# Kernel optimization log

Measured on AMD Instinct MI355X. Metric: run time of the kernel, lower is better.

The kernel has to match this reference:

```python
import jax, jax.numpy as jnp
import numpy as np

N_USERS = 100000
N_ITEMS = 50000
N = N_USERS + N_ITEMS + 2   # concat of user (+pad) and item (+pad) embedding tables
D = 128                      # embedding_size
E = 600000                   # edges per behavior adjacency
L = 2                        # GCN layers per (post, pre) behavior pair
EPS = 1e-12                  # F.normalize eps


def setup_inputs() -> dict:
    key = jax.random.key(0)
    ks = jax.random.split(key, 11)
    emb = jax.random.normal(ks[0], (N, D), jnp.float32) * 0.1
    rows_aux = jax.random.randint(ks[1], (E,), 0, N, jnp.int32)
    cols_aux = jax.random.randint(ks[2], (E,), 0, N, jnp.int32)
    vals_aux = jax.random.uniform(ks[3], (E,), jnp.float32)
    rows_buy = jax.random.randint(ks[4], (E,), 0, N, jnp.int32)
    cols_buy = jax.random.randint(ks[5], (E,), 0, N, jnp.int32)
    vals_buy = jax.random.uniform(ks[6], (E,), jnp.float32)
    trans_aux_all = jax.random.uniform(ks[7], (N, 1), jnp.float32)
    trans_buy_all = jax.random.uniform(ks[8], (N, 1), jnp.float32)
    trans_buy_aux = jax.random.uniform(ks[9], (N, 1), jnp.float32)
    # precomputed edge-dropout masks (keep_rate ~ 0.5 via 0/1 randint), one per SpMM layer call
    masks = jax.random.randint(ks[10], (6, E), 0, 2, jnp.int32).astype(bool)
    return {
        "emb": emb,
        "rows_aux": rows_aux, "cols_aux": cols_aux, "vals_aux": vals_aux,
        "rows_buy": rows_buy, "cols_buy": cols_buy, "vals_buy": vals_buy,
        "trans_aux_all": trans_aux_all,
        "trans_buy_all": trans_buy_all,
        "trans_buy_aux": trans_buy_aux,
        "masks": masks,
    }


def _spmm(rows, cols, vals, x):
    # sparse [N,N] @ dense [N,D] in COO form: gather source rows, scale, scatter-add to dest rows
    return jax.ops.segment_sum(vals[:, None] * x[cols], rows, num_segments=N)


def _gcn(x, rows, cols, vals, layer_masks):
    acc = x
    for l in range(L):
        x = _spmm(rows, cols, vals * layer_masks[l], x)
        acc = acc + x
    return acc / (L + 1)


def _l2norm(x):
    n = jnp.linalg.norm(x, axis=-1, keepdims=True)
    return x / jnp.maximum(n, EPS)


def reference(emb, rows_aux, cols_aux, vals_aux, rows_buy, cols_buy, vals_buy,
              trans_aux_all, trans_buy_all, trans_buy_aux, masks):
    m = masks.astype(emb.dtype)  # dropped edges contribute 0 == removing them from the COO tensor
    last = emb
    # behavior 'aux': pre-behaviors = ['all']
    g = _gcn(emb, rows_aux, cols_aux, vals_aux, m[0:2])
    agg = trans_aux_all * g
    cur_aux = _l2norm(agg) + last
    last = cur_aux
    # behavior 'buy': pre-behaviors = ['all', 'aux'] (reversed order; sum is order-invariant)
    g_all = _gcn(emb, rows_buy, cols_buy, vals_buy, m[2:4])
    g_aux = _gcn(cur_aux, rows_buy, cols_buy, vals_buy, m[4:6])
    agg = trans_buy_all * g_all + trans_buy_aux * g_aux
    cur_buy = _l2norm(agg) + last
    return cur_buy
```

## Files before the change

### kernel.cpp

```cpp
#include <hip/hip_runtime.h>
#include <cstdint>
#include <cstddef>

#define NNODES 150002
#define NN2    (2 * NNODES)
#define DIM    128
#define NEDGE  600000
#define EPSN   1e-12f


__global__ void hist_both(const int* __restrict__ ra,
                          const int* __restrict__ rb,
                          int* __restrict__ cnt)
{
    int e = blockIdx.x * blockDim.x + threadIdx.x;
    if (e < NEDGE)           atomicAdd(&cnt[ra[e]], 1);
    else if (e < 2 * NEDGE)  atomicAdd(&cnt[NNODES + rb[e - NEDGE]], 1);
}

__global__ __launch_bounds__(1024)
void scan_phase1(const int* __restrict__ cnt,
                 int* __restrict__ local,
                 int* __restrict__ partials)
{
    __shared__ int lds[1024];
    int t = threadIdx.x;
    int i = blockIdx.x * 1024 + t;
    int v = (i < NN2) ? cnt[i] : 0;
    lds[t] = v;
    __syncthreads();
    for (int off = 1; off < 1024; off <<= 1) {
        int w = (t >= off) ? lds[t - off] : 0;
        __syncthreads();
        lds[t] += w;
        __syncthreads();
    }
    if (i < NN2) local[i] = lds[t] - v;
    if (t == 1023) partials[blockIdx.x] = lds[1023];
}

__global__ __launch_bounds__(512)
void scan_phase2(int* __restrict__ partials, int nparts)
{
    __shared__ int lds[512];
    int t = threadIdx.x;
    int v = (t < nparts) ? partials[t] : 0;
    lds[t] = v;
    __syncthreads();
    for (int off = 1; off < 512; off <<= 1) {
        int w = (t >= off) ? lds[t - off] : 0;
        __syncthreads();
        lds[t] += w;
        __syncthreads();
    }
    if (t < nparts) partials[t] = lds[t] - v;
}

__global__ __launch_bounds__(1024)
void scan_phase3(int* __restrict__ rp,
                 const int* __restrict__ partials,
                 int* __restrict__ cursor)
{
    int i = blockIdx.x * 1024 + threadIdx.x;
    if (i >= NN2) return;
    int v = rp[i] + partials[blockIdx.x];
    rp[i] = v;
    cursor[i] = v;
    if (i == 0) rp[NN2] = 2 * NEDGE;
}

__global__ void scatter_both(const int* __restrict__ ra, const int* __restrict__ ca,
                             const float* __restrict__ va,
                             const int* __restrict__ rb, const int* __restrict__ cb,
                             const float* __restrict__ vb,
                             const int* __restrict__ masks,
                             int* __restrict__ cursor,
                             uint2* __restrict__ ent)
{
    int e = blockIdx.x * blockDim.x + threadIdx.x;
    if (e < NEDGE) {
        unsigned bits = (masks[e] != 0 ? 1u : 0u)
                      | (masks[(size_t)NEDGE + e] != 0 ? 2u : 0u);
        int pos = atomicAdd(&cursor[ra[e]], 1);
        ent[pos] = make_uint2((unsigned)ca[e] | (bits << 24), __float_as_uint(va[e]));
    } else if (e < 2 * NEDGE) {
        int e2 = e - NEDGE;
        unsigned bits = 0;
#pragma unroll
        for (int k = 0; k < 4; ++k)
            bits |= (masks[(size_t)(2 + k) * NEDGE + e2] != 0 ? 1u : 0u) << k;
        int pos = atomicAdd(&cursor[NNODES + rb[e2]], 1);
        ent[pos] = make_uint2((unsigned)cb[e2] | (bits << 24), __float_as_uint(vb[e2]));
    }
}

#define G16_SETUP                                              \
    int gid  = blockIdx.x * blockDim.x + threadIdx.x;          \
    int row  = gid >> 4;                                       \
    int lane = gid & 15;                                       \
    if (row >= NNODES) return;                                 \
    size_t base = (size_t)row * DIM + lane * 4;

#define FMA4(acc, v, xv)                                       \
    acc.x = fmaf(v, xv.x, acc.x);                              \
    acc.y = fmaf(v, xv.y, acc.y);                              \
    acc.z = fmaf(v, xv.z, acc.z);                              \
    acc.w = fmaf(v, xv.w, acc.w);

#define ADD4(a, b) a.x += b.x; a.y += b.y; a.z += b.z; a.w += b.w;

__device__ __forceinline__ void gather16_1(const int* __restrict__ rp,
                                           const uint2* __restrict__ ent,
                                           unsigned bm, int row, int lane,
                                           const float* __restrict__ x,
                                           float4& alo, float4& ahi)
{
    int j0 = rp[row], j1 = rp[row + 1];
    float4 l0 = {0,0,0,0}, h0 = {0,0,0,0}, l1 = {0,0,0,0}, h1 = {0,0,0,0};
    int j = j0;
    for (; j + 2 <= j1; j += 2) {
        uint2 Ea = ent[j], Eb = ent[j + 1];
        bool ma = (Ea.x & bm) != 0, mb = (Eb.x & bm) != 0;
        const float* pa = x + (size_t)(Ea.x & 0xFFFFFFu) * DIM + lane * 4;
        const float* pb = x + (size_t)(Eb.x & 0xFFFFFFu) * DIM + lane * 4;
        float4 xla, xha, xlb, xhb;
        if (ma) { xla = *(const float4*)pa;        xha = *(const float4*)(pa + 64); }
        if (mb) { xlb = *(const float4*)pb;        xhb = *(const float4*)(pb + 64); }
        if (ma) { float v = __uint_as_float(Ea.y); FMA4(l0, v, xla) FMA4(h0, v, xha) }
        if (mb) { float v = __uint_as_float(Eb.y); FMA4(l1, v, xlb) FMA4(h1, v, xhb) }
    }
    if (j < j1) {
        uint2 E = ent[j];
        if ((E.x & bm) != 0) {
            const float* p = x + (size_t)(E.x & 0xFFFFFFu) * DIM + lane * 4;
            float v = __uint_as_float(E.y);
            float4 xl = *(const float4*)p, xh = *(const float4*)(p + 64);
            FMA4(l0, v, xl) FMA4(h0, v, xh)
        }
    }
    ADD4(l0, l1) ADD4(h0, h1)
    alo = l0; ahi = h0;
}

__device__ __forceinline__ void gather16_2(const int* __restrict__ rp,
                                           const uint2* __restrict__ ent,
                                           int row, int lane,
                                           const float* __restrict__ xA, unsigned bmA,
                                           const float* __restrict__ xB, unsigned bmB,
                                           float4& Alo, float4& Ahi,
                                           float4& Blo, float4& Bhi)
{
    int j0 = rp[row], j1 = rp[row + 1];
    float4 al0 = {0,0,0,0}, ah0 = {0,0,0,0}, al1 = {0,0,0,0}, ah1 = {0,0,0,0};
    float4 bl0 = {0,0,0,0}, bh0 = {0,0,0,0}, bl1 = {0,0,0,0}, bh1 = {0,0,0,0};
    int j = j0;
    for (; j + 2 <= j1; j += 2) {
        uint2 Ea = ent[j], Eb = ent[j + 1];
        size_t ca = (size_t)(Ea.x & 0xFFFFFFu) * DIM + lane * 4;
        size_t cb = (size_t)(Eb.x & 0xFFFFFFu) * DIM + lane * 4;
        bool maA = (Ea.x & bmA) != 0, maB = (Ea.x & bmB) != 0;
        bool mbA = (Eb.x & bmA) != 0, mbB = (Eb.x & bmB) != 0;
        float4 xaAl, xaAh, xaBl, xaBh, xbAl, xbAh, xbBl, xbBh;
        if (maA) { xaAl = *(const float4*)(xA + ca); xaAh = *(const float4*)(xA + ca + 64); }
        if (maB) { xaBl = *(const float4*)(xB + ca); xaBh = *(const float4*)(xB + ca + 64); }
        if (mbA) { xbAl = *(const float4*)(xA + cb); xbAh = *(const float4*)(xA + cb + 64); }
        if (mbB) { xbBl = *(const float4*)(xB + cb); xbBh = *(const float4*)(xB + cb + 64); }
        float va = __uint_as_float(Ea.y), vb = __uint_as_float(Eb.y);
        if (maA) { FMA4(al0, va, xaAl) FMA4(ah0, va, xaAh) }
        if (maB) { FMA4(bl0, va, xaBl) FMA4(bh0, va, xaBh) }
        if (mbA) { FMA4(al1, vb, xbAl) FMA4(ah1, vb, xbAh) }
        if (mbB) { FMA4(bl1, vb, xbBl) FMA4(bh1, vb, xbBh) }
    }
    if (j < j1) {
        uint2 E = ent[j];
        size_t cc = (size_t)(E.x & 0xFFFFFFu) * DIM + lane * 4;
        bool mA = (E.x & bmA) != 0, mB = (E.x & bmB) != 0;
        float4 xAl, xAh, xBl, xBh;
        if (mA) { xAl = *(const float4*)(xA + cc); xAh = *(const float4*)(xA + cc + 64); }
        if (mB) { xBl = *(const float4*)(xB + cc); xBh = *(const float4*)(xB + cc + 64); }
        float v = __uint_as_float(E.y);
        if (mA) { FMA4(al0, v, xAl) FMA4(ah0, v, xAh) }
        if (mB) { FMA4(bl0, v, xBl) FMA4(bh0, v, xBh) }
    }
    ADD4(al0, al1) ADD4(ah0, ah1) ADD4(bl0, bl1) ADD4(bh0, bh1)
    Alo = al0; Ahi = ah0; Blo = bl0; Bhi = bh0;
}

__global__ void aux1_kernel(const int* __restrict__ rp, const uint2* __restrict__ ent,
                            const float* __restrict__ emb, float* __restrict__ B0)
{
    G16_SETUP
    float4 alo, ahi;
    gather16_1(rp, ent, 1u << 24, row, lane, emb, alo, ahi);
    *reinterpret_cast<float4*>(B0 + base)      = alo;
    *reinterpret_cast<float4*>(B0 + base + 64) = ahi;
}

__global__ void aux2_kernel(const int* __restrict__ rp, const uint2* __restrict__ ent,
                            const float* __restrict__ B0, const float* __restrict__ emb,
                            const float* __restrict__ trans, float* __restrict__ out)
{
    G16_SETUP
    float4 alo, ahi;
    gather16_1(rp, ent, 1u << 25, row, lane, B0, alo, ahi);
    float t = trans[row] * (1.0f / 3.0f);
    float4 elo = *reinterpret_cast<const float4*>(emb + base);
    float4 ehi = *reinterpret_cast<const float4*>(emb + base + 64);
    float4 blo = *reinterpret_cast<const float4*>(B0 + base);
    float4 bhi = *reinterpret_cast<const float4*>(B0 + base + 64);
    float4 lo, hi;
    lo.x = t * (elo.x + blo.x + alo.x); lo.y = t * (elo.y + blo.y + alo.y);
    lo.z = t * (elo.z + blo.z + alo.z); lo.w = t * (elo.w + blo.w + alo.w);
    hi.x = t * (ehi.x + bhi.x + ahi.x); hi.y = t * (ehi.y + bhi.y + ahi.y);
    hi.z = t * (ehi.z + bhi.z + ahi.z); hi.w = t * (ehi.w + bhi.w + ahi.w);
    float ss = lo.x*lo.x + lo.y*lo.y + lo.z*lo.z + lo.w*lo.w
             + hi.x*hi.x + hi.y*hi.y + hi.z*hi.z + hi.w*hi.w;
#pragma unroll
    for (int off = 8; off > 0; off >>= 1) ss += __shfl_xor(ss, off, 64);
    float inv = 1.0f / fmaxf(sqrtf(ss), EPSN);
    float4 olo, ohi;
    olo.x = lo.x * inv + elo.x; olo.y = lo.y * inv + elo.y;
    olo.z = lo.z * inv + elo.z; olo.w = lo.w * inv + elo.w;
    ohi.x = hi.x * inv + ehi.x; ohi.y = hi.y * inv + ehi.y;
    ohi.z = hi.z * inv + ehi.z; ohi.w = hi.w * inv + ehi.w;
    *reinterpret_cast<float4*>(out + base)      = olo;
    *reinterpret_cast<float4*>(out + base + 64) = ohi;
}

__global__ void buy1_kernel(const int* __restrict__ rp, const uint2* __restrict__ ent,
                            const float* __restrict__ emb, const float* __restrict__ cur,
                            float* __restrict__ B0, float* __restrict__ B1)
{
    G16_SETUP
    float4 Alo, Ahi, Xlo, Xhi;
    gather16_2(rp, ent, row, lane, emb, 1u << 24, cur, 1u << 26, Alo, Ahi, Xlo, Xhi);
    *reinterpret_cast<float4*>(B0 + base)      = Alo;
    *reinterpret_cast<float4*>(B0 + base + 64) = Ahi;
    *reinterpret_cast<float4*>(B1 + base)      = Xlo;
    *reinterpret_cast<float4*>(B1 + base + 64) = Xhi;
}

__global__ void buy2_kernel(const int* __restrict__ rp, const uint2* __restrict__ ent,
                            const float* __restrict__ B0, const float* __restrict__ B1,
                            const float* __restrict__ emb,
                            const float* __restrict__ tall, const float* __restrict__ taux,
                            float* __restrict__ out)
{
    G16_SETUP
    float4 Alo, Ahi, Xlo, Xhi;
    gather16_2(rp, ent, row, lane, B0, 1u << 25, B1, 1u << 27, Alo, Ahi, Xlo, Xhi);
    float ta = tall[row] * (1.0f / 3.0f);
    float tx = taux[row] * (1.0f / 3.0f);
    float4 elo = *reinterpret_cast<const float4*>(emb + base);
    float4 ehi = *reinterpret_cast<const float4*>(emb + base + 64);
    float4 clo = *reinterpret_cast<const float4*>(out + base);
    float4 chi = *reinterpret_cast<const float4*>(out + base + 64);
    float4 b0lo = *reinterpret_cast<const float4*>(B0 + base);
    float4 b0hi = *reinterpret_cast<const float4*>(B0 + base + 64);
    float4 b1lo = *reinterpret_cast<const float4*>(B1 + base);
    float4 b1hi = *reinterpret_cast<const float4*>(B1 + base + 64);
    float4 lo, hi;
    lo.x = ta * (elo.x + b0lo.x + Alo.x) + tx * (clo.x + b1lo.x + Xlo.x);
    lo.y = ta * (elo.y + b0lo.y + Alo.y) + tx * (clo.y + b1lo.y + Xlo.y);
    lo.z = ta * (elo.z + b0lo.z + Alo.z) + tx * (clo.z + b1lo.z + Xlo.z);
    lo.w = ta * (elo.w + b0lo.w + Alo.w) + tx * (clo.w + b1lo.w + Xlo.w);
    hi.x = ta * (ehi.x + b0hi.x + Ahi.x) + tx * (chi.x + b1hi.x + Xhi.x);
    hi.y = ta * (ehi.y + b0hi.y + Ahi.y) + tx * (chi.y + b1hi.y + Xhi.y);
    hi.z = ta * (ehi.z + b0hi.z + Ahi.z) + tx * (chi.z + b1hi.z + Xhi.z);
    hi.w = ta * (ehi.w + b0hi.w + Ahi.w) + tx * (chi.w + b1hi.w + Xhi.w);
    float ss = lo.x*lo.x + lo.y*lo.y + lo.z*lo.z + lo.w*lo.w
             + hi.x*hi.x + hi.y*hi.y + hi.z*hi.z + hi.w*hi.w;
#pragma unroll
    for (int off = 8; off > 0; off >>= 1) ss += __shfl_xor(ss, off, 64);
    float inv = 1.0f / fmaxf(sqrtf(ss), EPSN);
    float4 olo, ohi;
    olo.x = lo.x * inv + clo.x; olo.y = lo.y * inv + clo.y;
    olo.z = lo.z * inv + clo.z; olo.w = lo.w * inv + clo.w;
    ohi.x = hi.x * inv + chi.x; ohi.y = hi.y * inv + chi.y;
    ohi.z = hi.z * inv + chi.z; ohi.w = hi.w * inv + chi.w;
    *reinterpret_cast<float4*>(out + base)      = olo;
    *reinterpret_cast<float4*>(out + base + 64) = ohi;
}

__global__ void spmm_kernel(const int* __restrict__ rows, const int* __restrict__ cols,
                            const float* __restrict__ vals, const int* __restrict__ mask,
                            const float* __restrict__ x, float* __restrict__ y)
{
    long long gid = (long long)blockIdx.x * blockDim.x + threadIdx.x;
    int e = (int)(gid >> 5); int lane = (int)(gid & 31);
    if (e >= NEDGE) return;
    if (!mask[e]) return;
    float v = vals[e]; int c = cols[e]; int r = rows[e];
    float4 xv = *reinterpret_cast<const float4*>(x + (size_t)c * DIM + lane * 4);
    float* dst = y + (size_t)r * DIM + lane * 4;
    atomicAdd(dst + 0, v * xv.x); atomicAdd(dst + 1, v * xv.y);
    atomicAdd(dst + 2, v * xv.z); atomicAdd(dst + 3, v * xv.w);
}

__global__ void spmm_scaled_kernel(const int* __restrict__ rows, const int* __restrict__ cols,
                                   const float* __restrict__ vals, const int* __restrict__ mask,
                                   const float* __restrict__ x, float* __restrict__ y,
                                   const float* __restrict__ rowscale)
{
    long long gid = (long long)blockIdx.x * blockDim.x + threadIdx.x;
    int e = (int)(gid >> 5); int lane = (int)(gid & 31);
    if (e >= NEDGE) return;
    if (!mask[e]) return;
    int r = rows[e];
    float v = vals[e] * rowscale[r] * (1.0f / 3.0f);
    int c = cols[e];
    float4 xv = *reinterpret_cast<const float4*>(x + (size_t)c * DIM + lane * 4);
    float* dst = y + (size_t)r * DIM + lane * 4;
    atomicAdd(dst + 0, v * xv.x); atomicAdd(dst + 1, v * xv.y);
    atomicAdd(dst + 2, v * xv.z); atomicAdd(dst + 3, v * xv.w);
}

__global__ void rownorm_aux_kernel(const float* __restrict__ emb, const float* __restrict__ s,
                                   const float* __restrict__ trans, float* __restrict__ out)
{
    int gid = blockIdx.x * blockDim.x + threadIdx.x;
    int row = gid >> 6; int lane = gid & 63;
    if (row >= NNODES) return;
    float t = trans[row] * (1.0f / 3.0f);
    size_t base = (size_t)row * DIM + lane * 2;
    float2 e  = *reinterpret_cast<const float2*>(emb + base);
    float2 sv = *reinterpret_cast<const float2*>(s + base);
    float ax = t * (e.x + sv.x); float ay = t * (e.y + sv.y);
    float ss = ax * ax + ay * ay;
#pragma unroll
    for (int off = 32; off > 0; off >>= 1) ss += __shfl_xor(ss, off, 64);
    float inv = 1.0f / fmaxf(sqrtf(ss), EPSN);
    float2 o; o.x = ax * inv + e.x; o.y = ay * inv + e.y;
    *reinterpret_cast<float2*>(out + base) = o;
}

__global__ void rownorm_final_kernel(const float* __restrict__ cur_aux, const float* __restrict__ b,
                                     const float* __restrict__ tbaux, float* __restrict__ out)
{
    int gid = blockIdx.x * blockDim.x + threadIdx.x;
    int row = gid >> 6; int lane = gid & 63;
    if (row >= NNODES) return;
    float t = tbaux[row] * (1.0f / 3.0f);
    size_t base = (size_t)row * DIM + lane * 2;
    float2 ca = *reinterpret_cast<const float2*>(cur_aux + base);
    float2 bv = *reinterpret_cast<const float2*>(b + base);
    float ax = bv.x + t * ca.x; float ay = bv.y + t * ca.y;
    float ss = ax * ax + ay * ay;
#pragma unroll
    for (int off = 32; off > 0; off >>= 1) ss += __shfl_xor(ss, off, 64);
    float inv = 1.0f / fmaxf(sqrtf(ss), EPSN);
    float2 o; o.x = ax * inv + ca.x; o.y = ay * inv + ca.y;
    *reinterpret_cast<float2*>(out + base) = o;
}

__global__ void combine_all_kernel(const float* __restrict__ emb, const float* __restrict__ tball,
                                   float* __restrict__ b)
{
    int i = blockIdx.x * blockDim.x + threadIdx.x;
    const int n4 = NNODES * DIM / 4;
    if (i >= n4) return;
    int row = i >> 5;
    float t = tball[row] * (1.0f / 3.0f);
    float4 e  = reinterpret_cast<const float4*>(emb)[i];
    float4 bv = reinterpret_cast<float4*>(b)[i];
    bv.x = t * (e.x + bv.x); bv.y = t * (e.y + bv.y);
    bv.z = t * (e.z + bv.z); bv.w = t * (e.w + bv.w);
    reinterpret_cast<float4*>(b)[i] = bv;
}

__global__ void add_scaled_kernel(const float* __restrict__ a, const float* __restrict__ tbaux,
                                  float* __restrict__ b)
{
    int i = blockIdx.x * blockDim.x + threadIdx.x;
    const int n4 = NNODES * DIM / 4;
    if (i >= n4) return;
    int row = i >> 5;
    float t = tbaux[row] * (1.0f / 3.0f);
    float4 av = reinterpret_cast<const float4*>(a)[i];
    float4 bv = reinterpret_cast<float4*>(b)[i];
    bv.x += t * av.x; bv.y += t * av.y; bv.z += t * av.z; bv.w += t * av.w;
    reinterpret_cast<float4*>(b)[i] = bv;
}

extern "C" void kernel_launch(void* const* d_in, const int* in_sizes, int n_in,
                              void* d_out, int out_size, void* d_ws, size_t ws_size,
                              hipStream_t stream)
{
    const float* emb       = (const float*)d_in[0];
    const int*   rows_aux  = (const int*)d_in[1];
    const int*   cols_aux  = (const int*)d_in[2];
    const float* vals_aux  = (const float*)d_in[3];
    const int*   rows_buy  = (const int*)d_in[4];
    const int*   cols_buy  = (const int*)d_in[5];
    const float* vals_buy  = (const float*)d_in[6];
    const float* t_aux_all = (const float*)d_in[7];
    const float* t_buy_all = (const float*)d_in[8];
    const float* t_buy_aux = (const float*)d_in[9];
    const int*   masks     = (const int*)d_in[10];

    float* out = (float*)d_out;
    const size_t nd = (size_t)NNODES * DIM;
    const size_t nd_bytes = nd * sizeof(float);

    uint8_t* wsb = (uint8_t*)d_ws;
    size_t off = 0;
    auto carve = [&](size_t bytes) -> void* {
        void* p = wsb + off;
        off = (off + bytes + 15) & ~(size_t)15;
        return p;
    };
    const int SCAN_BLOCKS = (NN2 + 1023) / 1024;
    float* B0       = (float*)carve(nd_bytes);
    float* B1       = (float*)carve(nd_bytes);
    uint2* ent      = (uint2*)carve((size_t)2 * NEDGE * 8);
    int*   rp       = (int*)carve(((size_t)NN2 + 1) * 4);
    int*   cursor   = (int*)carve((size_t)NN2 * 4);
    int*   cnt      = (int*)carve((size_t)NN2 * 4);
    int*   partials = (int*)carve((size_t)SCAN_BLOCKS * 4);
    const bool use_csr = (off <= ws_size);

    if (use_csr) {
        const int EB   = 256;
        const int EG2  = (2 * NEDGE + EB - 1) / EB;
        const int GB   = 256;
        const int GG   = (NNODES * 16 + GB - 1) / GB;

        hipMemsetAsync(cnt, 0, (size_t)NN2 * 4, stream);
        hist_both<<<EG2, EB, 0, stream>>>(rows_aux, rows_buy, cnt);
        scan_phase1<<<SCAN_BLOCKS, 1024, 0, stream>>>(cnt, rp, partials);
        scan_phase2<<<1, 512, 0, stream>>>(partials, SCAN_BLOCKS);
        scan_phase3<<<SCAN_BLOCKS, 1024, 0, stream>>>(rp, partials, cursor);
        scatter_both<<<EG2, EB, 0, stream>>>(rows_aux, cols_aux, vals_aux,
                                             rows_buy, cols_buy, vals_buy,
                                             masks, cursor, ent);

        aux1_kernel<<<GG, GB, 0, stream>>>(rp, ent, emb, B0);
        aux2_kernel<<<GG, GB, 0, stream>>>(rp, ent, B0, emb, t_aux_all, out);

        buy1_kernel<<<GG, GB, 0, stream>>>(rp + NNODES, ent, emb, out, B0, B1);
        buy2_kernel<<<GG, GB, 0, stream>>>(rp + NNODES, ent, B0, B1, emb,
                                           t_buy_all, t_buy_aux, out);
        return;
    }

    const int SPMM_BLK  = 256;
    const int SPMM_GRID = (int)(((long long)NEDGE * 32 + SPMM_BLK - 1) / SPMM_BLK);
    const int ROW_BLK   = 256;
    const int ROW_GRID  = (NNODES * 64 + ROW_BLK - 1) / ROW_BLK;
    const int EW_BLK    = 256;
    const int EW_GRID   = (int)((nd / 4 + EW_BLK - 1) / EW_BLK);

    hipMemsetAsync(B0, 0, nd_bytes, stream);
    spmm_kernel<<<SPMM_GRID, SPMM_BLK, 0, stream>>>(rows_aux, cols_aux, vals_aux,
                                                    masks + 0 * (size_t)NEDGE, emb, B0);
    hipMemcpyAsync(B1, B0, nd_bytes, hipMemcpyDeviceToDevice, stream);
    spmm_kernel<<<SPMM_GRID, SPMM_BLK, 0, stream>>>(rows_aux, cols_aux, vals_aux,
                                                    masks + 1 * (size_t)NEDGE, B0, B1);
    rownorm_aux_kernel<<<ROW_GRID, ROW_BLK, 0, stream>>>(emb, B1, t_aux_all, out);

    hipMemsetAsync(B0, 0, nd_bytes, stream);
    spmm_kernel<<<SPMM_GRID, SPMM_BLK, 0, stream>>>(rows_buy, cols_buy, vals_buy,
                                                    masks + 2 * (size_t)NEDGE, emb, B0);
    hipMemcpyAsync(B1, B0, nd_bytes, hipMemcpyDeviceToDevice, stream);
    spmm_kernel<<<SPMM_GRID, SPMM_BLK, 0, stream>>>(rows_buy, cols_buy, vals_buy,
                                                    masks + 3 * (size_t)NEDGE, B0, B1);
    combine_all_kernel<<<EW_GRID, EW_BLK, 0, stream>>>(emb, t_buy_all, B1);

    hipMemsetAsync(B0, 0, nd_bytes, stream);
    spmm_kernel<<<SPMM_GRID, SPMM_BLK, 0, stream>>>(rows_buy, cols_buy, vals_buy,
                                                    masks + 4 * (size_t)NEDGE, out, B0);
    add_scaled_kernel<<<EW_GRID, EW_BLK, 0, stream>>>(B0, t_buy_aux, B1);
    spmm_scaled_kernel<<<SPMM_GRID, SPMM_BLK, 0, stream>>>(rows_buy, cols_buy, vals_buy,
                                                           masks + 5 * (size_t)NEDGE, B0, B1,
                                                           t_buy_aux);
    rownorm_final_kernel<<<ROW_GRID, ROW_BLK, 0, stream>>>(out, B1, t_buy_aux, out);
}
```

Before: 531.1 us.

## Store gathered embeddings and intermediates in bf16 to halve gather traffic

Adds a kernel that converts the embedding table to bf16, and stores the intermediate layer outputs (B0, B1, cur_aux copy) as bf16. The SpMM gather kernels then read 16 bytes per lane instead of 32, with fp32 accumulation. The goal is to cut memory bandwidth in the random-gather-bound CSR SpMM passes. In exchange it adds an extra conversion pass and loses precision in emb, intermediate layers and the self terms, which may hurt accuracy against the fp32 reference.

Measured after the change: 443.8 us. 16.4% less time.

```diff
diff --git a/kernel.cpp b/kernel.cpp
--- a/kernel.cpp
+++ b/kernel.cpp
@@ -8,6 +8,44 @@
 #define NEDGE  600000
 #define EPSN   1e-12f
 
+
+__device__ __forceinline__ float2 unpack_bf2(unsigned w)
+{
+    return make_float2(__uint_as_float(w << 16), __uint_as_float(w & 0xFFFF0000u));
+}
+
+__device__ __forceinline__ unsigned pack_bf2(float lo, float hi)
+{
+    unsigned ulo = __float_as_uint(lo); ulo += 0x7FFFu + ((ulo >> 16) & 1u);
+    unsigned uhi = __float_as_uint(hi); uhi += 0x7FFFu + ((uhi >> 16) & 1u);
+    return (ulo >> 16) | (uhi & 0xFFFF0000u);
+}
+
+__device__ __forceinline__ void fma8(float acc[8], float v, uint4 w)
+{
+    float2 p;
+    p = unpack_bf2(w.x); acc[0] = fmaf(v, p.x, acc[0]); acc[1] = fmaf(v, p.y, acc[1]);
+    p = unpack_bf2(w.y); acc[2] = fmaf(v, p.x, acc[2]); acc[3] = fmaf(v, p.y, acc[3]);
+    p = unpack_bf2(w.z); acc[4] = fmaf(v, p.x, acc[4]); acc[5] = fmaf(v, p.y, acc[5]);
+    p = unpack_bf2(w.w); acc[6] = fmaf(v, p.x, acc[6]); acc[7] = fmaf(v, p.y, acc[7]);
+}
+
+__device__ __forceinline__ void unpack8(float o[8], uint4 w)
+{
+    float2 p;
+    p = unpack_bf2(w.x); o[0] = p.x; o[1] = p.y;
+    p = unpack_bf2(w.y); o[2] = p.x; o[3] = p.y;
+    p = unpack_bf2(w.z); o[4] = p.x; o[5] = p.y;
+    p = unpack_bf2(w.w); o[6] = p.x; o[7] = p.y;
+}
+
+__device__ __forceinline__ uint4 pack8(const float o[8])
+{
+    uint4 w;
+    w.x = pack_bf2(o[0], o[1]); w.y = pack_bf2(o[2], o[3]);
+    w.z = pack_bf2(o[4], o[5]); w.w = pack_bf2(o[6], o[7]);
+    return w;
+}
 
 __global__ void hist_both(const int* __restrict__ ra,
                           const int* __restrict__ rb,
@@ -94,192 +132,178 @@
     }
 }
 
+__global__ void conv_bf16(const float* __restrict__ x, uint4* __restrict__ xbf)
+{
+    int i = blockIdx.x * blockDim.x + threadIdx.x;
+    const int n = NNODES * 16;
+    if (i >= n) return;
+    const float4* p = reinterpret_cast<const float4*>(x) + (size_t)i * 2;
+    float4 lo = p[0], hi = p[1];
+    uint4 w;
+    w.x = pack_bf2(lo.x, lo.y); w.y = pack_bf2(lo.z, lo.w);
+    w.z = pack_bf2(hi.x, hi.y); w.w = pack_bf2(hi.z, hi.w);
+    xbf[i] = w;
+}
+
 #define G16_SETUP                                              \
     int gid  = blockIdx.x * blockDim.x + threadIdx.x;          \
     int row  = gid >> 4;                                       \
     int lane = gid & 15;                                       \
-    if (row >= NNODES) return;                                 \
-    size_t base = (size_t)row * DIM + lane * 4;
-
-#define FMA4(acc, v, xv)                                       \
-    acc.x = fmaf(v, xv.x, acc.x);                              \
-    acc.y = fmaf(v, xv.y, acc.y);                              \
-    acc.z = fmaf(v, xv.z, acc.z);                              \
-    acc.w = fmaf(v, xv.w, acc.w);
-
-#define ADD4(a, b) a.x += b.x; a.y += b.y; a.z += b.z; a.w += b.w;
-
-__device__ __forceinline__ void gather16_1(const int* __restrict__ rp,
+    if (row >= NNODES) return;
+
+__device__ __forceinline__ void gatherbf_1(const int* __restrict__ rp,
                                            const uint2* __restrict__ ent,
                                            unsigned bm, int row, int lane,
-                                           const float* __restrict__ x,
-                                           float4& alo, float4& ahi)
+                                           const uint4* __restrict__ xbf,
+                                           float acc[8])
 {
     int j0 = rp[row], j1 = rp[row + 1];
-    float4 l0 = {0,0,0,0}, h0 = {0,0,0,0}, l1 = {0,0,0,0}, h1 = {0,0,0,0};
+    float a0[8] = {0,0,0,0,0,0,0,0}, a1[8] = {0,0,0,0,0,0,0,0};
     int j = j0;
     for (; j + 2 <= j1; j += 2) {
         uint2 Ea = ent[j], Eb = ent[j + 1];
         bool ma = (Ea.x & bm) != 0, mb = (Eb.x & bm) != 0;
-        const float* pa = x + (size_t)(Ea.x & 0xFFFFFFu) * DIM + lane * 4;
-        const float* pb = x + (size_t)(Eb.x & 0xFFFFFFu) * DIM + lane * 4;
-        float4 xla, xha, xlb, xhb;
-        if (ma) { xla = *(const float4*)pa;        xha = *(const float4*)(pa + 64); }
-        if (mb) { xlb = *(const float4*)pb;        xhb = *(const float4*)(pb + 64); }
-        if (ma) { float v = __uint_as_float(Ea.y); FMA4(l0, v, xla) FMA4(h0, v, xha) }
-        if (mb) { float v = __uint_as_float(Eb.y); FMA4(l1, v, xlb) FMA4(h1, v, xhb) }
+        uint4 wa, wb;
+        if (ma) wa = xbf[(size_t)(Ea.x & 0xFFFFFFu) * 16 + lane];
+        if (mb) wb = xbf[(size_t)(Eb.x & 0xFFFFFFu) * 16 + lane];
+        if (ma) fma8(a0, __uint_as_float(Ea.y), wa);
+        if (mb) fma8(a1, __uint_as_float(Eb.y), wb);
     }
     if (j < j1) {
         uint2 E = ent[j];
         if ((E.x & bm) != 0) {
-            const float* p = x + (size_t)(E.x & 0xFFFFFFu) * DIM + lane * 4;
-            float v = __uint_as_float(E.y);
-            float4 xl = *(const float4*)p, xh = *(const float4*)(p + 64);
-            FMA4(l0, v, xl) FMA4(h0, v, xh)
+            uint4 w = xbf[(size_t)(E.x & 0xFFFFFFu) * 16 + lane];
+            fma8(a0, __uint_as_float(E.y), w);
         }
     }
-    ADD4(l0, l1) ADD4(h0, h1)
-    alo = l0; ahi = h0;
-}
-
-__device__ __forceinline__ void gather16_2(const int* __restrict__ rp,
+#pragma unroll
+    for (int k = 0; k < 8; ++k) acc[k] = a0[k] + a1[k];
+}
+
+__device__ __forceinline__ void gatherbf_2(const int* __restrict__ rp,
                                            const uint2* __restrict__ ent,
                                            int row, int lane,
-                                           const float* __restrict__ xA, unsigned bmA,
-                                           const float* __restrict__ xB, unsigned bmB,
-                                           float4& Alo, float4& Ahi,
-                                           float4& Blo, float4& Bhi)
+                                           const uint4* __restrict__ xA, unsigned bmA,
+                                           const uint4* __restrict__ xB, unsigned bmB,
+                                           float accA[8], float accB[8])
 {
     int j0 = rp[row], j1 = rp[row + 1];
-    float4 al0 = {0,0,0,0}, ah0 = {0,0,0,0}, al1 = {0,0,0,0}, ah1 = {0,0,0,0};
-    float4 bl0 = {0,0,0,0}, bh0 = {0,0,0,0}, bl1 = {0,0,0,0}, bh1 = {0,0,0,0};
+#pragma unroll
+    for (int k = 0; k < 8; ++k) { accA[k] = 0.f; accB[k] = 0.f; }
     int j = j0;
     for (; j + 2 <= j1; j += 2) {
         uint2 Ea = ent[j], Eb = ent[j + 1];
-        size_t ca = (size_t)(Ea.x & 0xFFFFFFu) * DIM + lane * 4;
-        size_t cb = (size_t)(Eb.x & 0xFFFFFFu) * DIM + lane * 4;
+        size_t ia = (size_t)(Ea.x & 0xFFFFFFu) * 16 + lane;
+        size_t ib = (size_t)(Eb.x & 0xFFFFFFu) * 16 + lane;
         bool maA = (Ea.x & bmA) != 0, maB = (Ea.x & bmB) != 0;
         bool mbA = (Eb.x & bmA) != 0, mbB = (Eb.x & bmB) != 0;
-        float4 xaAl, xaAh, xaBl, xaBh, xbAl, xbAh, xbBl, xbBh;
-        if (maA) { xaAl = *(const float4*)(xA + ca); xaAh = *(const float4*)(xA + ca + 64); }
-        if (maB) { xaBl = *(const float4*)(xB + ca); xaBh = *(const float4*)(xB + ca + 64); }
-        if (mbA) { xbAl = *(const float4*)(xA + cb); xbAh = *(const float4*)(xA + cb + 64); }
-        if (mbB) { xbBl = *(const float4*)(xB + cb); xbBh = *(const float4*)(xB + cb + 64); }
+        uint4 waA, waB, wbA, wbB;
+        if (maA) waA = xA[ia];
+        if (maB) waB = xB[ia];
+        if (mbA) wbA = xA[ib];
+        if (mbB) wbB = xB[ib];
         float va = __uint_as_float(Ea.y), vb = __uint_as_float(Eb.y);
-        if (maA) { FMA4(al0, va, xaAl) FMA4(ah0, va, xaAh) }
-        if (maB) { FMA4(bl0, va, xaBl) FMA4(bh0, va, xaBh) }
-        if (mbA) { FMA4(al1, vb, xbAl) FMA4(ah1, vb, xbAh) }
-        if (mbB) { FMA4(bl1, vb, xbBl) FMA4(bh1, vb, xbBh) }
+        if (maA) fma8(accA, va, waA);
+        if (maB) fma8(accB, va, waB);
+        if (mbA) fma8(accA, vb, wbA);
+        if (mbB) fma8(accB, vb, wbB);
     }
     if (j < j1) {
         uint2 E = ent[j];
-        size_t cc = (size_t)(E.x & 0xFFFFFFu) * DIM + lane * 4;
+        size_t ic = (size_t)(E.x & 0xFFFFFFu) * 16 + lane;
         bool mA = (E.x & bmA) != 0, mB = (E.x & bmB) != 0;
-        float4 xAl, xAh, xBl, xBh;
-        if (mA) { xAl = *(const float4*)(xA + cc); xAh = *(const float4*)(xA + cc + 64); }
-        if (mB) { xBl = *(const float4*)(xB + cc); xBh = *(const float4*)(xB + cc + 64); }
+        uint4 wA, wB;
+        if (mA) wA = xA[ic];
+        if (mB) wB = xB[ic];
         float v = __uint_as_float(E.y);
-        if (mA) { FMA4(al0, v, xAl) FMA4(ah0, v, xAh) }
-        if (mB) { FMA4(bl0, v, xBl) FMA4(bh0, v, xBh) }
-    }
-    ADD4(al0, al1) ADD4(ah0, ah1) ADD4(bl0, bl1) ADD4(bh0, bh1)
-    Alo = al0; Ahi = ah0; Blo = bl0; Bhi = bh0;
+        if (mA) fma8(accA, v, wA);
+        if (mB) fma8(accB, v, wB);
+    }
 }
 
 __global__ void aux1_kernel(const int* __restrict__ rp, const uint2* __restrict__ ent,
-                            const float* __restrict__ emb, float* __restrict__ B0)
+                            const uint4* __restrict__ Ebf, uint4* __restrict__ B0bf)
 {
     G16_SETUP
-    float4 alo, ahi;
-    gather16_1(rp, ent, 1u << 24, row, lane, emb, alo, ahi);
-    *reinterpret_cast<float4*>(B0 + base)      = alo;
-    *reinterpret_cast<float4*>(B0 + base + 64) = ahi;
+    float acc[8];
+    gatherbf_1(rp, ent, 1u << 24, row, lane, Ebf, acc);
+    B0bf[(size_t)row * 16 + lane] = pack8(acc);
 }
 
 __global__ void aux2_kernel(const int* __restrict__ rp, const uint2* __restrict__ ent,
-                            const float* __restrict__ B0, const float* __restrict__ emb,
-                            const float* __restrict__ trans, float* __restrict__ out)
+                            const uint4* __restrict__ B0bf, const uint4* __restrict__ Ebf,
+                            const float* __restrict__ trans,
+                            float* __restrict__ out, uint4* __restrict__ Cbf)
 {
     G16_SETUP
-    float4 alo, ahi;
-    gather16_1(rp, ent, 1u << 25, row, lane, B0, alo, ahi);
+    float acc[8];
+    gatherbf_1(rp, ent, 1u << 25, row, lane, B0bf, acc);
+    size_t ri = (size_t)row * 16 + lane;
+    float e8[8], b8[8];
+    unpack8(e8, Ebf[ri]);
+    unpack8(b8, B0bf[ri]);
     float t = trans[row] * (1.0f / 3.0f);
-    float4 elo = *reinterpret_cast<const float4*>(emb + base);
-    float4 ehi = *reinterpret_cast<const float4*>(emb + base + 64);
-    float4 blo = *reinterpret_cast<const float4*>(B0 + base);
-    float4 bhi = *reinterpret_cast<const float4*>(B0 + base + 64);
-    float4 lo, hi;
-    lo.x = t * (elo.x + blo.x + alo.x); lo.y = t * (elo.y + blo.y + alo.y);
-    lo.z = t * (elo.z + blo.z + alo.z); lo.w = t * (elo.w + blo.w + alo.w);
-    hi.x = t * (ehi.x + bhi.x + ahi.x); hi.y = t * (ehi.y + bhi.y + ahi.y);
-    hi.z = t * (ehi.z + bhi.z + ahi.z); hi.w = t * (ehi.w + bhi.w + ahi.w);
-    float ss = lo.x*lo.x + lo.y*lo.y + lo.z*lo.z + lo.w*lo.w
-             + hi.x*hi.x + hi.y*hi.y + hi.z*hi.z + hi.w*hi.w;
+    float a[8], ss = 0.f;
+#pragma unroll
+    for (int k = 0; k < 8; ++k) { a[k] = t * (e8[k] + b8[k] + acc[k]); ss += a[k] * a[k]; }
 #pragma unroll
     for (int off = 8; off > 0; off >>= 1) ss += __shfl_xor(ss, off, 64);
     float inv = 1.0f / fmaxf(sqrtf(ss), EPSN);
-    float4 olo, ohi;
-    olo.x = lo.x * inv + elo.x; olo.y = lo.y * inv + elo.y;
-    olo.z = lo.z * inv + elo.z; olo.w = lo.w * inv + elo.w;
-    ohi.x = hi.x * inv + ehi.x; ohi.y = hi.y * inv + ehi.y;
-    ohi.z = hi.z * inv + ehi.z; ohi.w = hi.w * inv + ehi.w;
-    *reinterpret_cast<float4*>(out + base)      = olo;
-    *reinterpret_cast<float4*>(out + base + 64) = ohi;
+    float o[8];
+#pragma unroll
+    for (int k = 0; k < 8; ++k) o[k] = a[k] * inv + e8[k];
+    float* op = out + (size_t)row * DIM + lane * 8;
+    *reinterpret_cast<float4*>(op)     = make_float4(o[0], o[1], o[2], o[3]);
+    *reinterpret_cast<float4*>(op + 4) = make_float4(o[4], o[5], o[6], o[7]);
+    Cbf[ri] = pack8(o);
 }
 
 __global__ void buy1_kernel(const int* __restrict__ rp, const uint2* __restrict__ ent,
-                            const float* __restrict__ emb, const float* __restrict__ cur,
-                            float* __restrict__ B0, float* __restrict__ B1)
+                            const uint4* __restrict__ Ebf, const uint4* __restrict__ Cbf,
+                            uint4* __restrict__ B0bf, uint4* __restrict__ B1bf)
 {
     G16_SETUP
-    float4 Alo, Ahi, Xlo, Xhi;
-    gather16_2(rp, ent, row, lane, emb, 1u << 24, cur, 1u << 26, Alo, Ahi, Xlo, Xhi);
-    *reinterpret_cast<float4*>(B0 + base)      = Alo;
-    *reinterpret_cast<float4*>(B0 + base + 64) = Ahi;
-    *reinterpret_cast<float4*>(B1 + base)      = Xlo;
-    *reinterpret_cast<float4*>(B1 + base + 64) = Xhi;
+    float accA[8], accX[8];
+    gatherbf_2(rp, ent, row, lane, Ebf, 1u << 24, Cbf, 1u << 26, accA, accX);
+    size_t ri = (size_t)row * 16 + lane;
+    B0bf[ri] = pack8(accA);
+    B1bf[ri] = pack8(accX);
 }
 
 __global__ void buy2_kernel(const int* __restrict__ rp, const uint2* __restrict__ ent,
-                            const float* __restrict__ B0, const float* __restrict__ B1,
-                            const float* __restrict__ emb,
+                            const uint4* __restrict__ B0bf, const uint4* __restrict__ B1bf,
+                            const uint4* __restrict__ Ebf,
                             const float* __restrict__ tall, const float* __restrict__ taux,
                             float* __restrict__ out)
 {
     G16_SETUP
-    float4 Alo, Ahi, Xlo, Xhi;
-    gather16_2(rp, ent, row, lane, B0, 1u << 25, B1, 1u << 27, Alo, Ahi, Xlo, Xhi);
+    float accA[8], accX[8];
+    gatherbf_2(rp, ent, row, lane, B0bf, 1u << 25, B1bf, 1u << 27, accA, accX);
+    size_t ri = (size_t)row * 16 + lane;
+    float e8[8], b0[8], b1[8];
+    unpack8(e8, Ebf[ri]);
+    unpack8(b0, B0bf[ri]);
+    unpack8(b1, B1bf[ri]);
+    float* op = out + (size_t)row * DIM + lane * 8;
+    float4 c0 = *reinterpret_cast<const float4*>(op);
+    float4 c1 = *reinterpret_cast<const float4*>(op + 4);
+    float c8[8] = {c0.x, c0.y, c0.z, c0.w, c1.x, c1.y, c1.z, c1.w};
     float ta = tall[row] * (1.0f / 3.0f);
     float tx = taux[row] * (1.0f / 3.0f);
-    float4 elo = *reinterpret_cast<const float4*>(emb + base);
-    float4 ehi = *reinterpret_cast<const float4*>(emb + base + 64);
-    float4 clo = *reinterpret_cast<const float4*>(out + base);
-    float4 chi = *reinterpret_cast<const float4*>(out + base + 64);
-    float4 b0lo = *reinterpret_cast<const float4*>(B0 + base);
-    float4 b0hi = *reinterpret_cast<const float4*>(B0 + base + 64);
-    float4 b1lo = *reinterpret_cast<const float4*>(B1 + base);
-    float4 b1hi = *reinterpret_cast<const float4*>(B1 + base + 64);
-    float4 lo, hi;
-    lo.x = ta * (elo.x + b0lo.x + Alo.x) + tx * (clo.x + b1lo.x + Xlo.x);
-    lo.y = ta * (elo.y + b0lo.y + Alo.y) + tx * (clo.y + b1lo.y + Xlo.y);
-    lo.z = ta * (elo.z + b0lo.z + Alo.z) + tx * (clo.z + b1lo.z + Xlo.z);
-    lo.w = ta * (elo.w + b0lo.w + Alo.w) + tx * (clo.w + b1lo.w + Xlo.w);
-    hi.x = ta * (ehi.x + b0hi.x + Ahi.x) + tx * (chi.x + b1hi.x + Xhi.x);
-    hi.y = ta * (ehi.y + b0hi.y + Ahi.y) + tx * (chi.y + b1hi.y + Xhi.y);
-    hi.z = ta * (ehi.z + b0hi.z + Ahi.z) + tx * (chi.z + b1hi.z + Xhi.z);
-    hi.w = ta * (ehi.w + b0hi.w + Ahi.w) + tx * (chi.w + b1hi.w + Xhi.w);
-    float ss = lo.x*lo.x + lo.y*lo.y + lo.z*lo.z + lo.w*lo.w
-             + hi.x*hi.x + hi.y*hi.y + hi.z*hi.z + hi.w*hi.w;
+    float a[8], ss = 0.f;
+#pragma unroll
+    for (int k = 0; k < 8; ++k) {
+        a[k] = ta * (e8[k] + b0[k] + accA[k]) + tx * (c8[k] + b1[k] + accX[k]);
+        ss += a[k] * a[k];
+    }
 #pragma unroll
     for (int off = 8; off > 0; off >>= 1) ss += __shfl_xor(ss, off, 64);
     float inv = 1.0f / fmaxf(sqrtf(ss), EPSN);
-    float4 olo, ohi;
-    olo.x = lo.x * inv + clo.x; olo.y = lo.y * inv + clo.y;
-    olo.z = lo.z * inv + clo.z; olo.w = lo.w * inv + clo.w;
-    ohi.x = hi.x * inv + chi.x; ohi.y = hi.y * inv + chi.y;
-    ohi.z = hi.z * inv + chi.z; ohi.w = hi.w * inv + chi.w;
-    *reinterpret_cast<float4*>(out + base)      = olo;
-    *reinterpret_cast<float4*>(out + base + 64) = ohi;
+    float o[8];
+#pragma unroll
+    for (int k = 0; k < 8; ++k) o[k] = a[k] * inv + c8[k];
+    *reinterpret_cast<float4*>(op)     = make_float4(o[0], o[1], o[2], o[3]);
+    *reinterpret_cast<float4*>(op + 4) = make_float4(o[4], o[5], o[6], o[7]);
 }
 
 __global__ void spmm_kernel(const int* __restrict__ rows, const int* __restrict__ cols,
@@ -401,6 +425,7 @@
     float* out = (float*)d_out;
     const size_t nd = (size_t)NNODES * DIM;
     const size_t nd_bytes = nd * sizeof(float);
+    const size_t bf_bytes = nd * 2;
 
     uint8_t* wsb = (uint8_t*)d_ws;
     size_t off = 0;
@@ -410,8 +435,10 @@
         return p;
     };
     const int SCAN_BLOCKS = (NN2 + 1023) / 1024;
-    float* B0       = (float*)carve(nd_bytes);
-    float* B1       = (float*)carve(nd_bytes);
+    uint4* Ebf      = (uint4*)carve(bf_bytes);
+    uint4* B0bf     = (uint4*)carve(bf_bytes);
+    uint4* B1bf     = (uint4*)carve(bf_bytes);
+    uint4* Cbf      = (uint4*)carve(bf_bytes);
     uint2* ent      = (uint2*)carve((size_t)2 * NEDGE * 8);
     int*   rp       = (int*)carve(((size_t)NN2 + 1) * 4);
     int*   cursor   = (int*)carve((size_t)NN2 * 4);
@@ -424,6 +451,8 @@
         const int EG2  = (2 * NEDGE + EB - 1) / EB;
         const int GB   = 256;
         const int GG   = (NNODES * 16 + GB - 1) / GB;
+
+        conv_bf16<<<GG, GB, 0, stream>>>(emb, Ebf);
 
         hipMemsetAsync(cnt, 0, (size_t)NN2 * 4, stream);
         hist_both<<<EG2, EB, 0, stream>>>(rows_aux, rows_buy, cnt);
@@ -434,14 +463,17 @@
                                              rows_buy, cols_buy, vals_buy,
                                              masks, cursor, ent);
 
-        aux1_kernel<<<GG, GB, 0, stream>>>(rp, ent, emb, B0);
-        aux2_kernel<<<GG, GB, 0, stream>>>(rp, ent, B0, emb, t_aux_all, out);
-
-        buy1_kernel<<<GG, GB, 0, stream>>>(rp + NNODES, ent, emb, out, B0, B1);
-        buy2_kernel<<<GG, GB, 0, stream>>>(rp + NNODES, ent, B0, B1, emb,
+        aux1_kernel<<<GG, GB, 0, stream>>>(rp, ent, Ebf, B0bf);
+        aux2_kernel<<<GG, GB, 0, stream>>>(rp, ent, B0bf, Ebf, t_aux_all, out, Cbf);
+
+        buy1_kernel<<<GG, GB, 0, stream>>>(rp + NNODES, ent, Ebf, Cbf, B0bf, B1bf);
+        buy2_kernel<<<GG, GB, 0, stream>>>(rp + NNODES, ent, B0bf, B1bf, Ebf,
                                            t_buy_all, t_buy_aux, out);
         return;
     }
+
+    float* B0 = (float*)d_ws;
+    float* B1 = B0 + nd;
 
     const int SPMM_BLK  = 256;
     const int SPMM_GRID = (int)(((long long)NEDGE * 32 + SPMM_BLK - 1) / SPMM_BLK);
```
